# Kernel tuning notes

Measured on AMD Instinct MI355X. Metric: run time of the kernel, lower is better.

Reference implementation:

```python
import jax, jax.numpy as jnp
import numpy as np
import math

N_EMBD = 1024
N_HEADS = 16
B, T = 4, 2048

def setup_inputs() -> dict:
    key = jax.random.key(0)
    k1, k2, k3 = jax.random.split(key, 3)
    x = jax.random.normal(k1, (B, T, N_EMBD), dtype=jnp.float32)
    scale = 1.0 / math.sqrt(N_EMBD)
    W_attn = jax.random.normal(k2, (N_EMBD, 3 * N_EMBD), dtype=jnp.float32) * scale
    W_proj = jax.random.normal(k3, (N_EMBD, N_EMBD), dtype=jnp.float32) * scale
    return {"x": x, "W_attn": W_attn, "W_proj": W_proj}

def reference(x, W_attn, W_proj):
    Bb, Tt, C = x.shape
    hd = C // N_HEADS
    qkv = x @ W_attn  # [B,T,3C]
    q, k, v = jnp.split(qkv, 3, axis=-1)
    # [B,H,T,hd]
    q = q.reshape(Bb, Tt, N_HEADS, hd).transpose(0, 2, 1, 3)
    k = k.reshape(Bb, Tt, N_HEADS, hd).transpose(0, 2, 1, 3)
    v = v.reshape(Bb, Tt, N_HEADS, hd).transpose(0, 2, 1, 3)
    att = jnp.einsum('bhqd,bhkd->bhqk', q, k) * (1.0 / math.sqrt(hd))
    mask = jnp.tril(jnp.ones((Tt, Tt), dtype=bool))
    att = jnp.where(mask[None, None], att, -jnp.inf)
    att = jax.nn.softmax(att, axis=-1)
    out = jnp.einsum('bhqk,bhkd->bhqd', att, v)
    out = out.transpose(0, 2, 1, 3).reshape(Bb, Tt, C)
    return out @ W_proj
```

## Files before the change

kernel.cpp:

```cpp
#include <hip/hip_runtime.h>
#include <cstddef>
#include <cstdint>

typedef __attribute__((ext_vector_type(8))) _Float16 half8;
typedef __attribute__((ext_vector_type(4))) _Float16 half4;
typedef __attribute__((ext_vector_type(4))) float f32x4;
typedef __attribute__((ext_vector_type(16))) float f32x16;

#define N_EMBD 1024
#define N_HEADS 16
#define BATCH 4
#define SEQ 2048
#define C3 3072
#define HD 64

__device__ inline uint32_t pk2(float x, float y) {
    auto h2 = __builtin_amdgcn_cvt_pkrtz(x, y);
    uint32_t u;
    __builtin_memcpy(&u, &h2, 4);
    return u;
}

__device__ inline void swap32(uint32_t& a, uint32_t& b) {
    asm volatile("v_permlane32_swap_b32 %0, %1" : "+v"(a), "+v"(b));
}

__global__ void cvt_f32_f16(const float* __restrict__ in, _Float16* __restrict__ out, int n) {
    int i = (blockIdx.x * 256 + threadIdx.x) * 4;
    if (i >= n) return;
    float4 v = *(const float4*)(in + i);
    half4 h;
    h[0] = (_Float16)v.x; h[1] = (_Float16)v.y; h[2] = (_Float16)v.z; h[3] = (_Float16)v.w;
    *(half4*)(out + i) = h;
}

__global__ void transpose_cvt(const float* __restrict__ in, _Float16* __restrict__ out,
                              int R, int Ncols) {
    __shared__ float tile[32][33];
    int n0 = blockIdx.x * 32, r0 = blockIdx.y * 32;
    int tx = threadIdx.x, ty = threadIdx.y;
#pragma unroll
    for (int i = 0; i < 32; i += 8)
        tile[ty + i][tx] = in[(size_t)(r0 + ty + i) * Ncols + n0 + tx];
    __syncthreads();
#pragma unroll
    for (int i = 0; i < 32; i += 8)
        out[(size_t)(n0 + ty + i) * R + r0 + tx] = (_Float16)tile[tx][ty + i];
}

__global__ void transpose_v(const _Float16* __restrict__ qkv, _Float16* __restrict__ vT) {
    __shared__ _Float16 tile[32][36];
    int t0 = blockIdx.x * 32;
    int bhd = blockIdx.y;
    int bh = bhd >> 1, dh = bhd & 1;
    int b = bh >> 4, h = bh & 15;
    int tx = threadIdx.x, ty = threadIdx.y;
#pragma unroll
    for (int i = 0; i < 32; i += 8)
        tile[ty + i][tx] = qkv[(size_t)(b * SEQ + t0 + ty + i) * C3 + 2 * N_EMBD + h * HD + dh * 32 + tx];
    __syncthreads();
#pragma unroll
    for (int i = 0; i < 32; i += 8)
        vT[((size_t)bh * HD + dh * 32 + ty + i) * SEQ + t0 + tx] = tile[tx][ty + i];
}

__device__ inline void store1(float* p, float v) { *p = v; }
__device__ inline void store1(_Float16* p, float v) { *p = (_Float16)v; }

template <typename OutT>
__global__ __launch_bounds__(512, 1) void gemm192(
    const _Float16* __restrict__ A, const _Float16* __restrict__ Bt,
    OutT* __restrict__ C, int M, int N, int K) {
    __shared__ _Float16 Al[2][256 * 64];
    __shared__ _Float16 Bl[2][192 * 64];
    const int tid = threadIdx.x;
    const int lane = tid & 63, wave = tid >> 6;
    const int l15 = lane & 15, l4 = lane >> 4;
    const int wm = wave >> 2, wn = wave & 3;

    const int nwg = gridDim.x, nbx = N / 192;
    int wg = blockIdx.x;
    if ((nwg & 7) == 0) { int cpx = nwg >> 3; wg = (wg & 7) * cpx + (wg >> 3); }
    const int row0 = (wg / nbx) * 256, col0 = (wg % nbx) * 192;
    const int TAU = K >> 6;

    const int srow = tid >> 3, su = tid & 7;
    const int usrc8 = (su ^ (srow & 7)) * 8;
    auto stageAu = [&](int unit, int ts) {
        __builtin_amdgcn_global_load_lds(
            (const __attribute__((address_space(1))) void*)(A + (size_t)(row0 + unit * 64 + srow) * K + ts * 64 + usrc8),
            (__attribute__((address_space(3))) void*)(&Al[ts & 1][unit * 64 * 64 + tid * 8]), 16, 0, 0);
    };
    auto stageBu = [&](int unit, int ts) {
        __builtin_amdgcn_global_load_lds(
            (const __attribute__((address_space(1))) void*)(Bt + (size_t)(col0 + unit * 64 + srow) * K + ts * 64 + usrc8),
            (__attribute__((address_space(3))) void*)(&Bl[ts & 1][unit * 64 * 64 + tid * 8]), 16, 0, 0);
    };
    auto stageTile = [&](int ts) {
        stageAu(0, ts); stageAu(1, ts); stageAu(2, ts); stageAu(3, ts);
        stageBu(0, ts); stageBu(1, ts); stageBu(2, ts);
    };

    f32x4 acc[8][3] = {};
    stageTile(0); stageTile(1);
    asm volatile("s_waitcnt vmcnt(7)" ::: "memory");
    __builtin_amdgcn_s_barrier();

    half8 a[4][2], b[3][2];
    for (int tau = 0; tau < TAU; ++tau) {
        const _Float16* Ab = &Al[tau & 1][0];
        const _Float16* Bb = &Bl[tau & 1][0];
        const bool t2 = (tau + 2 < TAU);

#pragma unroll
        for (int m = 0; m < 4; ++m)
#pragma unroll
            for (int ks = 0; ks < 2; ++ks) {
                int r = wm * 128 + m * 16 + l15;
                a[m][ks] = *(const half8*)(Ab + r * 64 + (((ks * 4 + l4) ^ (r & 7)) * 8));
            }
#pragma unroll
        for (int n = 0; n < 3; ++n)
#pragma unroll
            for (int ks = 0; ks < 2; ++ks) {
                int r = wn * 48 + n * 16 + l15;
                b[n][ks] = *(const half8*)(Bb + r * 64 + (((ks * 4 + l4) ^ (r & 7)) * 8));
            }
        __builtin_amdgcn_s_barrier();
        __builtin_amdgcn_s_setprio(1);
#pragma unroll
        for (int m = 0; m < 4; ++m)
#pragma unroll
            for (int n = 0; n < 2; ++n)
#pragma unroll
                for (int ks = 0; ks < 2; ++ks)
                    acc[m][n] = __builtin_amdgcn_mfma_f32_16x16x32_f16(a[m][ks], b[n][ks], acc[m][n], 0, 0, 0);
        __builtin_amdgcn_s_setprio(0);
        __builtin_amdgcn_s_barrier();

        if (t2) { stageBu(0, tau + 2); stageBu(1, tau + 2); stageBu(2, tau + 2); }
        __builtin_amdgcn_s_barrier();
        __builtin_amdgcn_s_setprio(1);
#pragma unroll
        for (int m = 0; m < 4; ++m)
#pragma unroll
            for (int ks = 0; ks < 2; ++ks)
                acc[m][2] = __builtin_amdgcn_mfma_f32_16x16x32_f16(a[m][ks], b[2][ks], acc[m][2], 0, 0, 0);
        __builtin_amdgcn_s_setprio(0);
        __builtin_amdgcn_s_barrier();

#pragma unroll
        for (int m = 0; m < 4; ++m)
#pragma unroll
            for (int ks = 0; ks < 2; ++ks) {
                int r = wm * 128 + 64 + m * 16 + l15;
                a[m][ks] = *(const half8*)(Ab + r * 64 + (((ks * 4 + l4) ^ (r & 7)) * 8));
            }
        if (t2) { stageAu(0, tau + 2); stageAu(2, tau + 2); }
        __builtin_amdgcn_s_barrier();
        __builtin_amdgcn_s_setprio(1);
#pragma unroll
        for (int m = 0; m < 4; ++m)
#pragma unroll
            for (int n = 0; n < 2; ++n)
#pragma unroll
                for (int ks = 0; ks < 2; ++ks)
                    acc[4 + m][n] = __builtin_amdgcn_mfma_f32_16x16x32_f16(a[m][ks], b[n][ks], acc[4 + m][n], 0, 0, 0);
        __builtin_amdgcn_s_setprio(0);
        __builtin_amdgcn_s_barrier();

        if (t2) { stageAu(1, tau + 2); stageAu(3, tau + 2); }
        __builtin_amdgcn_s_barrier();
        __builtin_amdgcn_s_setprio(1);
#pragma unroll
        for (int m = 0; m < 4; ++m)
#pragma unroll
            for (int ks = 0; ks < 2; ++ks)
                acc[4 + m][2] = __builtin_amdgcn_mfma_f32_16x16x32_f16(a[m][ks], b[2][ks], acc[4 + m][2], 0, 0, 0);
        __builtin_amdgcn_s_setprio(0);
        if (tau <= TAU - 3) {
            asm volatile("s_waitcnt vmcnt(7)" ::: "memory");
        } else if (tau == TAU - 2) {
            asm volatile("s_waitcnt vmcnt(0)" ::: "memory");
        }
        __builtin_amdgcn_s_barrier();
    }

#pragma unroll
    for (int mi = 0; mi < 8; ++mi)
#pragma unroll
        for (int ni = 0; ni < 3; ++ni)
#pragma unroll
            for (int j = 0; j < 4; ++j) {
                int r = row0 + wm * 128 + (mi >> 2) * 64 + (mi & 3) * 16 + l4 * 4 + j;
                int c = col0 + wn * 48 + ni * 16 + l15;
                store1(C + (size_t)r * N + c, acc[mi][ni][j]);
            }
}

template <typename OutT>
__global__ __launch_bounds__(256, 2) void gemm_h(
    const _Float16* __restrict__ A, const _Float16* __restrict__ Bt,
    OutT* __restrict__ C, int M, int N, int K) {
    __shared__ _Float16 Al[128 * 32];
    __shared__ _Float16 Bl[128 * 32];
    const int tid = threadIdx.x;
    const int wave = tid >> 6, lane = tid & 63;
    const int l15 = lane & 15, l4 = lane >> 4;
    const int gx = gridDim.x;
    int lin = blockIdx.y * gx + blockIdx.x;
    int bcol, brow;
    if ((gx & 7) == 0) {
        int cpx = gx >> 3;
        int xcd = lin & 7;
        int idx = lin >> 3;
        bcol = xcd * cpx + idx % cpx;
        brow = idx / cpx;
    } else { bcol = blockIdx.x; brow = blockIdx.y; }
    const int row0 = brow * 128, col0 = bcol * 128;
    const int wm = wave >> 1, wn = wave & 1;
    f32x4 acc[4][4] = {};
    for (int k0 = 0; k0 < K; k0 += 32) {
#pragma unroll
        for (int i = 0; i < 2; ++i) {
            int c = tid + 256 * i;
            int r = c >> 2, c8 = (c & 3) * 8;
            __builtin_amdgcn_global_load_lds(
                (const __attribute__((address_space(1))) void*)(A + (size_t)(row0 + r) * K + k0 + c8),
                (__attribute__((address_space(3))) void*)(Al + (size_t)(wave * 64 + 256 * i) * 8),
                16, 0, 0);
        }
#pragma unroll
        for (int i = 0; i < 2; ++i) {
            int c = tid + 256 * i;
            int r = c >> 2, c8 = (c & 3) * 8;
            __builtin_amdgcn_global_load_lds(
                (const __attribute__((address_space(1))) void*)(Bt + (size_t)(col0 + r) * K + k0 + c8),
                (__attribute__((address_space(3))) void*)(Bl + (size_t)(wave * 64 + 256 * i) * 8),
                16, 0, 0);
        }
        __syncthreads();
        half8 a[4], b[4];
#pragma unroll
        for (int m = 0; m < 4; ++m)
            a[m] = *(const half8*)(Al + (wm * 64 + m * 16 + l15) * 32 + l4 * 8);
#pragma unroll
        for (int n = 0; n < 4; ++n)
            b[n] = *(const half8*)(Bl + (wn * 64 + n * 16 + l15) * 32 + l4 * 8);
        __builtin_amdgcn_s_setprio(1);
#pragma unroll
        for (int m = 0; m < 4; ++m)
#pragma unroll
            for (int n = 0; n < 4; ++n)
                acc[m][n] = __builtin_amdgcn_mfma_f32_16x16x32_f16(a[m], b[n], acc[m][n], 0, 0, 0);
        __builtin_amdgcn_s_setprio(0);
        __syncthreads();
    }
#pragma unroll
    for (int m = 0; m < 4; ++m)
#pragma unroll
        for (int n = 0; n < 4; ++n)
#pragma unroll
            for (int j = 0; j < 4; ++j) {
                int r = row0 + wm * 64 + m * 16 + l4 * 4 + j;
                int cc = col0 + wn * 64 + n * 16 + l15;
                store1(C + (size_t)r * N + cc, acc[m][n][j]);
            }
}

__global__ __launch_bounds__(256, 2) void attn_kernel(const _Float16* __restrict__ qkv,
                                                      const _Float16* __restrict__ vT,
                                                      _Float16* __restrict__ ao) {
    const int bid = blockIdx.x;
    const int qt = 15 - (bid >> 6);
    const int bh = bid & 63;
    const int b = bh >> 4, h = bh & 15;
    const int tid = threadIdx.x, lane = tid & 63;
    const int wave = tid >> 6;
    const int l31 = lane & 31, L = lane >> 5;

    __shared__ _Float16 Kl[4][64 * 64];
    __shared__ _Float16 Vl[4][64 * 64];

    const float qscale = 0.125f * 1.44269504089f;
    const float NEGC = -4.0f * 1.44269504089f;

    const int q0w = qt * 128 + wave * 32;
    const int q_g = q0w + l31;
    const int nt = 2 * qt + 2;

    auto stage = [&](int t, int buf) {
#pragma unroll
        for (int i = 0; i < 2; ++i) {
            int idx = tid + 256 * i;
            int key = idx >> 3, u = idx & 7;
            int d8 = (u ^ (key & 7)) * 8;
            __builtin_amdgcn_global_load_lds(
                (const __attribute__((address_space(1))) void*)(qkv + (size_t)(b * SEQ + t * 64 + key) * C3 + N_EMBD + h * HD + d8),
                (__attribute__((address_space(3))) void*)(&Kl[buf][idx * 8]), 16, 0, 0);
        }
#pragma unroll
        for (int i = 0; i < 2; ++i) {
            int idx = tid + 256 * i;
            int d = idx >> 3, u = idx & 7;
            int k8 = (u ^ (d & 7)) * 8;
            __builtin_amdgcn_global_load_lds(
                (const __attribute__((address_space(1))) void*)(vT + ((size_t)bh * HD + d) * SEQ + t * 64 + k8),
                (__attribute__((address_space(3))) void*)(&Vl[buf][idx * 8]), 16, 0, 0);
        }
    };

    stage(0, 0);
    stage(1, 1);

    half8 qb[4];
#pragma unroll
    for (int ks = 0; ks < 4; ++ks) {
        half8 v = *(const half8*)(qkv + (size_t)(b * SEQ + q_g) * C3 + h * HD + ks * 16 + L * 8);
#pragma unroll
        for (int e = 0; e < 8; ++e) v[e] = (_Float16)((float)v[e] * qscale);
        qb[ks] = v;
    }
    half8 onesf;
#pragma unroll
    for (int e = 0; e < 8; ++e) onesf[e] = (_Float16)1.0f;

    const f32x16 cinit = (f32x16)(NEGC);
    f32x16 o[2];
    o[0] = (f32x16)(0.f);
    o[1] = (f32x16)(0.f);
    f32x16 lac = (f32x16)(0.f);
    f32x16 sE[2], sO[2];

    auto qk = [&](int t, f32x16 (&s)[2]) {
        if (t * 64 > q0w + 31) return;
        const _Float16* Kb = &Kl[t & 3][0];
        __builtin_amdgcn_s_setprio(1);
#pragma unroll
        for (int kb = 0; kb < 2; ++kb) {
            const int key = kb * 32 + l31;
            {
                half8 kf = *(const half8*)(Kb + key * 64 + ((L ^ (key & 7)) * 8));
                s[kb] = __builtin_amdgcn_mfma_f32_32x32x16_f16(kf, qb[0], cinit, 0, 0, 0);
            }
#pragma unroll
            for (int ks = 1; ks < 4; ++ks) {
                half8 kf = *(const half8*)(Kb + key * 64 + (((ks * 2 + L) ^ (key & 7)) * 8));
                s[kb] = __builtin_amdgcn_mfma_f32_32x32x16_f16(kf, qb[ks], s[kb], 0, 0, 0);
            }
        }
        __builtin_amdgcn_s_setprio(0);
    };

    auto finish = [&](int t, f32x16 (&s)[2]) {
        if (t * 64 > q0w + 31) return;
        const int kv0 = t * 64;
        const _Float16* Vb = &Vl[t & 3][0];
        const bool needmask = (kv0 + 63 > q0w);
#pragma unroll
        for (int kb = 0; kb < 2; ++kb) {
#pragma unroll
            for (int r = 0; r < 16; ++r) {
                float v = exp2f(s[kb][r]);
                if (needmask) {
                    int key_g = kv0 + kb * 32 + (r & 3) + 8 * (r >> 2) + 4 * L;
                    v = (key_g > q_g) ? 0.f : v;
                }
                s[kb][r] = v;
            }
        }
        half8 paf[4];
#pragma unroll
        for (int kb = 0; kb < 2; ++kb)
#pragma unroll
            for (int hf = 0; hf < 2; ++hf) {
                const int bse = hf * 8;
                uint32_t a0 = pk2(s[kb][bse + 0], s[kb][bse + 1]);
                uint32_t b0 = pk2(s[kb][bse + 4], s[kb][bse + 5]);
                swap32(a0, b0);
                uint32_t a1 = pk2(s[kb][bse + 2], s[kb][bse + 3]);
                uint32_t b1 = pk2(s[kb][bse + 6], s[kb][bse + 7]);
                swap32(a1, b1);
                uint32_t w[4] = {a0, a1, b0, b1};
                __builtin_memcpy(&paf[kb * 2 + hf], w, 16);
            }
        __builtin_amdgcn_s_setprio(1);
#pragma unroll
        for (int ks = 0; ks < 4; ++ks) {
            lac = __builtin_amdgcn_mfma_f32_32x32x16_f16(paf[ks], onesf, lac, 0, 0, 0);
#pragma unroll
            for (int db = 0; db < 2; ++db) {
                const int d = db * 32 + l31;
                half8 vb = *(const half8*)(Vb + d * 64 + (((ks * 2 + L) ^ (d & 7)) * 8));
                o[db] = __builtin_amdgcn_mfma_f32_32x32x16_f16(paf[ks], vb, o[db], 0, 0, 0);
            }
        }
        __builtin_amdgcn_s_setprio(0);
    };

    asm volatile("s_waitcnt vmcnt(8)" ::: "memory");
    __builtin_amdgcn_s_barrier();

    if (nt > 2) stage(2, 2);
    qk(0, sE);
    if (nt > 2) { asm volatile("s_waitcnt vmcnt(4)" ::: "memory"); }
    else        { asm volatile("s_waitcnt vmcnt(0)" ::: "memory"); }
    __builtin_amdgcn_s_barrier();

    int u = 1;
    for (; u + 1 < nt; u += 2) {
        if (u + 2 < nt) stage(u + 2, (u + 2) & 3);
        qk(u, sO);
        finish(u - 1, sE);
        if (u + 2 < nt) { asm volatile("s_waitcnt vmcnt(4)" ::: "memory"); }
        else            { asm volatile("s_waitcnt vmcnt(0)" ::: "memory"); }
        __builtin_amdgcn_s_barrier();
        if (u + 3 < nt) stage(u + 3, (u + 3) & 3);
        qk(u + 1, sE);
        finish(u, sO);
        if (u + 3 < nt) { asm volatile("s_waitcnt vmcnt(4)" ::: "memory"); }
        else            { asm volatile("s_waitcnt vmcnt(0)" ::: "memory"); }
        __builtin_amdgcn_s_barrier();
    }
    qk(nt - 1, sO);
    finish(nt - 2, sE);
    finish(nt - 1, sO);

#pragma unroll
    for (int db = 0; db < 2; ++db)
#pragma unroll
        for (int r = 0; r < 16; ++r) {
            int qg = q0w + (r & 3) + 8 * (r >> 2) + 4 * L;
            ao[(size_t)(b * SEQ + qg) * N_EMBD + h * HD + db * 32 + l31] =
                (_Float16)(o[db][r] / lac[r]);
        }
}

extern "C" void kernel_launch(void* const* d_in, const int* in_sizes, int n_in,
                              void* d_out, int out_size, void* d_ws, size_t ws_size,
                              hipStream_t stream) {
    const float* x  = (const float*)d_in[0];
    const float* Wa = (const float*)d_in[1];
    const float* Wp = (const float*)d_in[2];
    float* out = (float*)d_out;

    const int M = BATCH * SEQ;
    _Float16* xh  = (_Float16*)d_ws;
    _Float16* WaT = xh + (size_t)M * N_EMBD;
    _Float16* WpT = WaT + (size_t)C3 * N_EMBD;
    _Float16* qkv = WpT + (size_t)N_EMBD * N_EMBD;
    _Float16* ao  = qkv + (size_t)M * C3;
    _Float16* vT  = xh;

    int nx = M * N_EMBD;
    cvt_f32_f16<<<nx / 4 / 256, 256, 0, stream>>>(x, xh, nx);
    dim3 tb(32, 8);
    transpose_cvt<<<dim3(C3 / 32, N_EMBD / 32), tb, 0, stream>>>(Wa, WaT, N_EMBD, C3);
    transpose_cvt<<<dim3(N_EMBD / 32, N_EMBD / 32), tb, 0, stream>>>(Wp, WpT, N_EMBD, N_EMBD);

    gemm192<_Float16><<<dim3((M / 256) * (C3 / 192)), 512, 0, stream>>>(xh, WaT, qkv, M, C3, N_EMBD);

    transpose_v<<<dim3(SEQ / 32, BATCH * N_HEADS * 2), tb, 0, stream>>>(qkv, vT);

    attn_kernel<<<dim3(1024), 256, 0, stream>>>(qkv, vT, ao);

    gemm_h<float><<<dim3(N_EMBD / 128, M / 128), 256, 0, stream>>>(ao, WpT, out, M, N_EMBD, N_EMBD);
}
```

Baseline: 194.3 us.

## Triple-buffer GEMM K-loop; simplify attention to double-buffered loop with higher occupancy

The fp16 GEMM gets a three-stage LDS ring with two tiles in flight and a single barrier per K step, replacing the load-sync-compute-sync loop so global loads overlap MFMA work. The attention kernel drops its four-buffer, software-pipelined QK/PV interleave in favour of a plain double-buffered loop. It shrinks LDS to 32 KB per block and raises launch bounds to 4 blocks per CU. The attention change trades intra-wave overlap of QK with softmax/PV for more resident waves, and waits vmcnt(0) every tile.

```diff
diff --git a/kernel.cpp b/kernel.cpp
--- a/kernel.cpp
+++ b/kernel.cpp
@@ -202,8 +202,8 @@
 __global__ __launch_bounds__(256, 2) void gemm_h(
     const _Float16* __restrict__ A, const _Float16* __restrict__ Bt,
     OutT* __restrict__ C, int M, int N, int K) {
-    __shared__ _Float16 Al[128 * 32];
-    __shared__ _Float16 Bl[128 * 32];
+    __shared__ _Float16 Al[3][128 * 32];
+    __shared__ _Float16 Bl[3][128 * 32];
     const int tid = threadIdx.x;
     const int wave = tid >> 6, lane = tid & 63;
     const int l15 = lane & 15, l4 = lane >> 4;
@@ -219,15 +219,16 @@
     } else { bcol = blockIdx.x; brow = blockIdx.y; }
     const int row0 = brow * 128, col0 = bcol * 128;
     const int wm = wave >> 1, wn = wave & 1;
-    f32x4 acc[4][4] = {};
-    for (int k0 = 0; k0 < K; k0 += 32) {
+    const int TAU = K >> 5;
+
+    auto stageT = [&](int ts, int buf) {
 #pragma unroll
         for (int i = 0; i < 2; ++i) {
             int c = tid + 256 * i;
             int r = c >> 2, c8 = (c & 3) * 8;
             __builtin_amdgcn_global_load_lds(
-                (const __attribute__((address_space(1))) void*)(A + (size_t)(row0 + r) * K + k0 + c8),
-                (__attribute__((address_space(3))) void*)(Al + (size_t)(wave * 64 + 256 * i) * 8),
+                (const __attribute__((address_space(1))) void*)(A + (size_t)(row0 + r) * K + ts * 32 + c8),
+                (__attribute__((address_space(3))) void*)(&Al[buf][(size_t)(wave * 64 + 256 * i) * 8]),
                 16, 0, 0);
         }
 #pragma unroll
@@ -235,18 +236,28 @@
             int c = tid + 256 * i;
             int r = c >> 2, c8 = (c & 3) * 8;
             __builtin_amdgcn_global_load_lds(
-                (const __attribute__((address_space(1))) void*)(Bt + (size_t)(col0 + r) * K + k0 + c8),
-                (__attribute__((address_space(3))) void*)(Bl + (size_t)(wave * 64 + 256 * i) * 8),
+                (const __attribute__((address_space(1))) void*)(Bt + (size_t)(col0 + r) * K + ts * 32 + c8),
+                (__attribute__((address_space(3))) void*)(&Bl[buf][(size_t)(wave * 64 + 256 * i) * 8]),
                 16, 0, 0);
         }
-        __syncthreads();
+    };
+
+    f32x4 acc[4][4] = {};
+    stageT(0, 0); stageT(1, 1);
+    asm volatile("s_waitcnt vmcnt(4)" ::: "memory");
+    __builtin_amdgcn_s_barrier();
+
+    int cur = 0;
+    for (int t = 0; t < TAU; ++t) {
+        int sb = cur + 2; if (sb >= 3) sb -= 3;
+        if (t + 2 < TAU) stageT(t + 2, sb);
         half8 a[4], b[4];
 #pragma unroll
         for (int m = 0; m < 4; ++m)
-            a[m] = *(const half8*)(Al + (wm * 64 + m * 16 + l15) * 32 + l4 * 8);
+            a[m] = *(const half8*)(&Al[cur][(wm * 64 + m * 16 + l15) * 32 + l4 * 8]);
 #pragma unroll
         for (int n = 0; n < 4; ++n)
-            b[n] = *(const half8*)(Bl + (wn * 64 + n * 16 + l15) * 32 + l4 * 8);
+            b[n] = *(const half8*)(&Bl[cur][(wn * 64 + n * 16 + l15) * 32 + l4 * 8]);
         __builtin_amdgcn_s_setprio(1);
 #pragma unroll
         for (int m = 0; m < 4; ++m)
@@ -254,7 +265,13 @@
             for (int n = 0; n < 4; ++n)
                 acc[m][n] = __builtin_amdgcn_mfma_f32_16x16x32_f16(a[m], b[n], acc[m][n], 0, 0, 0);
         __builtin_amdgcn_s_setprio(0);
-        __syncthreads();
+        if (t + 2 < TAU) {
+            asm volatile("s_waitcnt vmcnt(4)" ::: "memory");
+        } else if (t + 1 < TAU) {
+            asm volatile("s_waitcnt vmcnt(0)" ::: "memory");
+        }
+        __builtin_amdgcn_s_barrier();
+        ++cur; if (cur == 3) cur = 0;
     }
 #pragma unroll
     for (int m = 0; m < 4; ++m)
@@ -268,7 +285,7 @@
             }
 }
 
-__global__ __launch_bounds__(256, 2) void attn_kernel(const _Float16* __restrict__ qkv,
+__global__ __launch_bounds__(256, 4) void attn_kernel(const _Float16* __restrict__ qkv,
                                                       const _Float16* __restrict__ vT,
                                                       _Float16* __restrict__ ao) {
     const int bid = blockIdx.x;
@@ -279,8 +296,8 @@
     const int wave = tid >> 6;
     const int l31 = lane & 31, L = lane >> 5;
 
-    __shared__ _Float16 Kl[4][64 * 64];
-    __shared__ _Float16 Vl[4][64 * 64];
+    __shared__ _Float16 Kl[2][64 * 64];
+    __shared__ _Float16 Vl[2][64 * 64];
 
     const float qscale = 0.125f * 1.44269504089f;
     const float NEGC = -4.0f * 1.44269504089f;
@@ -311,7 +328,6 @@
     };
 
     stage(0, 0);
-    stage(1, 1);
 
     half8 qb[4];
 #pragma unroll
@@ -330,101 +346,80 @@
     o[0] = (f32x16)(0.f);
     o[1] = (f32x16)(0.f);
     f32x16 lac = (f32x16)(0.f);
-    f32x16 sE[2], sO[2];
-
-    auto qk = [&](int t, f32x16 (&s)[2]) {
-        if (t * 64 > q0w + 31) return;
-        const _Float16* Kb = &Kl[t & 3][0];
-        __builtin_amdgcn_s_setprio(1);
-#pragma unroll
-        for (int kb = 0; kb < 2; ++kb) {
-            const int key = kb * 32 + l31;
-            {
-                half8 kf = *(const half8*)(Kb + key * 64 + ((L ^ (key & 7)) * 8));
-                s[kb] = __builtin_amdgcn_mfma_f32_32x32x16_f16(kf, qb[0], cinit, 0, 0, 0);
-            }
-#pragma unroll
-            for (int ks = 1; ks < 4; ++ks) {
-                half8 kf = *(const half8*)(Kb + key * 64 + (((ks * 2 + L) ^ (key & 7)) * 8));
-                s[kb] = __builtin_amdgcn_mfma_f32_32x32x16_f16(kf, qb[ks], s[kb], 0, 0, 0);
-            }
-        }
-        __builtin_amdgcn_s_setprio(0);
-    };
-
-    auto finish = [&](int t, f32x16 (&s)[2]) {
-        if (t * 64 > q0w + 31) return;
+
+    asm volatile("s_waitcnt vmcnt(0)" ::: "memory");
+    __builtin_amdgcn_s_barrier();
+
+    for (int t = 0; t < nt; ++t) {
+        const int cur = t & 1;
         const int kv0 = t * 64;
-        const _Float16* Vb = &Vl[t & 3][0];
-        const bool needmask = (kv0 + 63 > q0w);
-#pragma unroll
-        for (int kb = 0; kb < 2; ++kb) {
-#pragma unroll
-            for (int r = 0; r < 16; ++r) {
-                float v = exp2f(s[kb][r]);
-                if (needmask) {
-                    int key_g = kv0 + kb * 32 + (r & 3) + 8 * (r >> 2) + 4 * L;
-                    v = (key_g > q_g) ? 0.f : v;
+        const bool pf = (t + 1 < nt);
+        if (pf) stage(t + 1, cur ^ 1);
+
+        if (kv0 <= q0w + 31) {
+            const _Float16* Kb = &Kl[cur][0];
+            const _Float16* Vb = &Vl[cur][0];
+            f32x16 s[2];
+            __builtin_amdgcn_s_setprio(1);
+#pragma unroll
+            for (int kb = 0; kb < 2; ++kb) {
+                const int key = kb * 32 + l31;
+                {
+                    half8 kf = *(const half8*)(Kb + key * 64 + ((L ^ (key & 7)) * 8));
+                    s[kb] = __builtin_amdgcn_mfma_f32_32x32x16_f16(kf, qb[0], cinit, 0, 0, 0);
                 }
-                s[kb][r] = v;
-            }
-        }
-        half8 paf[4];
-#pragma unroll
-        for (int kb = 0; kb < 2; ++kb)
-#pragma unroll
-            for (int hf = 0; hf < 2; ++hf) {
-                const int bse = hf * 8;
-                uint32_t a0 = pk2(s[kb][bse + 0], s[kb][bse + 1]);
-                uint32_t b0 = pk2(s[kb][bse + 4], s[kb][bse + 5]);
-                swap32(a0, b0);
-                uint32_t a1 = pk2(s[kb][bse + 2], s[kb][bse + 3]);
-                uint32_t b1 = pk2(s[kb][bse + 6], s[kb][bse + 7]);
-                swap32(a1, b1);
-                uint32_t w[4] = {a0, a1, b0, b1};
-                __builtin_memcpy(&paf[kb * 2 + hf], w, 16);
-            }
-        __builtin_amdgcn_s_setprio(1);
-#pragma unroll
-        for (int ks = 0; ks < 4; ++ks) {
-            lac = __builtin_amdgcn_mfma_f32_32x32x16_f16(paf[ks], onesf, lac, 0, 0, 0);
-#pragma unroll
-            for (int db = 0; db < 2; ++db) {
-                const int d = db * 32 + l31;
-                half8 vb = *(const half8*)(Vb + d * 64 + (((ks * 2 + L) ^ (d & 7)) * 8));
-                o[db] = __builtin_amdgcn_mfma_f32_32x32x16_f16(paf[ks], vb, o[db], 0, 0, 0);
-            }
-        }
-        __builtin_amdgcn_s_setprio(0);
-    };
-
-    asm volatile("s_waitcnt vmcnt(8)" ::: "memory");
-    __builtin_amdgcn_s_barrier();
-
-    if (nt > 2) stage(2, 2);
-    qk(0, sE);
-    if (nt > 2) { asm volatile("s_waitcnt vmcnt(4)" ::: "memory"); }
-    else        { asm volatile("s_waitcnt vmcnt(0)" ::: "memory"); }
-    __builtin_amdgcn_s_barrier();
-
-    int u = 1;
-    for (; u + 1 < nt; u += 2) {
-        if (u + 2 < nt) stage(u + 2, (u + 2) & 3);
-        qk(u, sO);
-        finish(u - 1, sE);
-        if (u + 2 < nt) { asm volatile("s_waitcnt vmcnt(4)" ::: "memory"); }
-        else            { asm volatile("s_waitcnt vmcnt(0)" ::: "memory"); }
-        __builtin_amdgcn_s_barrier();
-        if (u + 3 < nt) stage(u + 3, (u + 3) & 3);
-        qk(u + 1, sE);
-        finish(u, sO);
-        if (u + 3 < nt) { asm volatile("s_waitcnt vmcnt(4)" ::: "memory"); }
-        else            { asm volatile("s_waitcnt vmcnt(0)" ::: "memory"); }
+#pragma unroll
+                for (int ks = 1; ks < 4; ++ks) {
+                    half8 kf = *(const half8*)(Kb + key * 64 + (((ks * 2 + L) ^ (key & 7)) * 8));
+                    s[kb] = __builtin_amdgcn_mfma_f32_32x32x16_f16(kf, qb[ks], s[kb], 0, 0, 0);
+                }
+            }
+            __builtin_amdgcn_s_setprio(0);
+            const bool needmask = (kv0 + 63 > q0w);
+#pragma unroll
+            for (int kb = 0; kb < 2; ++kb) {
+#pragma unroll
+                for (int r = 0; r < 16; ++r) {
+                    float v = exp2f(s[kb][r]);
+                    if (needmask) {
+                        int key_g = kv0 + kb * 32 + (r & 3) + 8 * (r >> 2) + 4 * L;
+                        v = (key_g > q_g) ? 0.f : v;
+                    }
+                    s[kb][r] = v;
+                }
+            }
+            half8 paf[4];
+#pragma unroll
+            for (int kb = 0; kb < 2; ++kb)
+#pragma unroll
+                for (int hf = 0; hf < 2; ++hf) {
+                    const int bse = hf * 8;
+                    uint32_t a0 = pk2(s[kb][bse + 0], s[kb][bse + 1]);
+                    uint32_t b0 = pk2(s[kb][bse + 4], s[kb][bse + 5]);
+                    swap32(a0, b0);
+                    uint32_t a1 = pk2(s[kb][bse + 2], s[kb][bse + 3]);
+                    uint32_t b1 = pk2(s[kb][bse + 6], s[kb][bse + 7]);
+                    swap32(a1, b1);
+                    uint32_t w[4] = {a0, a1, b0, b1};
+                    __builtin_memcpy(&paf[kb * 2 + hf], w, 16);
+                }
+            __builtin_amdgcn_s_setprio(1);
+#pragma unroll
+            for (int ks = 0; ks < 4; ++ks) {
+                lac = __builtin_amdgcn_mfma_f32_32x32x16_f16(paf[ks], onesf, lac, 0, 0, 0);
+#pragma unroll
+                for (int db = 0; db < 2; ++db) {
+                    const int d = db * 32 + l31;
+                    half8 vb = *(const half8*)(Vb + d * 64 + (((ks * 2 + L) ^ (d & 7)) * 8));
+                    o[db] = __builtin_amdgcn_mfma_f32_32x32x16_f16(paf[ks], vb, o[db], 0, 0, 0);
+                }
+            }
+            __builtin_amdgcn_s_setprio(0);
+        }
+
+        if (pf) { asm volatile("s_waitcnt vmcnt(0)" ::: "memory"); }
         __builtin_amdgcn_s_barrier();
     }
-    qk(nt - 1, sO);
-    finish(nt - 2, sE);
-    finish(nt - 1, sO);
 
 #pragma unroll
     for (int db = 0; db < 2; ++db)
```

Measured after the change: 200.0 us. 1.03x slower.
